# Performance work log

Hardware: AMD Instinct MI355X
Metric: run time of the kernel (lower is better)

Reference implementation:

```python
import jax, jax.numpy as jnp
import numpy as np

# SNNConfig constants (see init_kwargs)
TAU_MEM = 0.02
TAU_SYN = 0.005
DT = 0.001
THRESHOLD = 1.0
BETA = 10.0  # fast-sigmoid surrogate beta

BATCH, TIME, IN_DIM, HIDDEN = 32, 1024, 512, 512


@jax.custom_vjp
def spike_fn(v):
    """Heaviside spike with fast-sigmoid surrogate gradient."""
    return (v > THRESHOLD).astype(v.dtype)


def _spike_fwd(v):
    return spike_fn(v), v


def _spike_bwd(v, g):
    x = v - THRESHOLD
    surr = 1.0 / jnp.square(1.0 + BETA * jnp.abs(x))
    return (g * surr,)


spike_fn.defvjp(_spike_fwd, _spike_bwd)


def setup_inputs() -> dict:
    key = jax.random.key(0)
    k1, k2 = jax.random.split(key)
    spikes = jax.random.uniform(k1, (BATCH, TIME, IN_DIM), dtype=jnp.float32)
    # xavier_uniform for (IN_DIM, HIDDEN)
    limit = np.sqrt(6.0 / (IN_DIM + HIDDEN))
    W = jax.random.uniform(k2, (IN_DIM, HIDDEN), dtype=jnp.float32,
                           minval=-limit, maxval=limit)
    b = jnp.zeros((HIDDEN,), dtype=jnp.float32)
    return {"spikes": spikes, "W": W, "b": b}


def reference(spikes, W, b):
    # spikes: [B, T, I]; W: [I, H]; b: [H]
    alpha_mem = jnp.exp(jnp.asarray(-DT / TAU_MEM, dtype=spikes.dtype))
    alpha_syn = jnp.exp(jnp.asarray(-DT / TAU_SYN, dtype=spikes.dtype))
    # hoist the per-step GEMM into one big contraction: [B, T, H]
    I_in = jnp.einsum('bti,ih->bth', spikes, W) + b

    B, T, H = I_in.shape
    v0 = jnp.zeros((B, H), dtype=spikes.dtype)
    s0 = jnp.zeros((B, H), dtype=spikes.dtype)

    def lif_step(carry, i_t):
        v_mem, i_syn = carry
        i_syn = alpha_syn * i_syn + i_t
        v_mem = alpha_mem * v_mem + i_syn
        out = spike_fn(v_mem)
        v_mem = v_mem - out * THRESHOLD  # soft reset
        return (v_mem, i_syn), out

    _, out_spikes = jax.lax.scan(lif_step, (v0, s0), I_in.transpose(1, 0, 2))
    return out_spikes.transpose(1, 0, 2)  # [B, T, H]
```

## Files before the change

kernel.cpp:

```cpp
#include <hip/hip_runtime.h>
#include <hip/hip_bf16.h>

constexpr int BATCH  = 32;
constexpr int TIME   = 1024;
constexpr int IN_DIM = 512;
constexpr int HIDDEN = 512;

constexpr int GM = BATCH * TIME;
constexpr int GN = HIDDEN;
constexpr int GK = IN_DIM;

#define GLOBAL_AS __attribute__((address_space(1)))
#define LDS_AS    __attribute__((address_space(3)))

#define WAITCNT_VMCNT(n) (((n) & 15) | (((n) >> 4) << 14) | (0x7 << 4) | (0xF << 8))
#define COMPILER_FENCE() asm volatile("" ::: "memory")

constexpr int BM = 128;
constexpr int BN = 128;
constexpr int BK = 16;
constexpr int LDAs = BM + 4;
constexpr int LDBs = BN + 4;

__global__ __launch_bounds__(256) void sgemm_bias_kernel(
    const float* __restrict__ A,
    const float* __restrict__ B,
    const float* __restrict__ bias,
    float* __restrict__ C)
{
    __shared__ __align__(16) float As[BK * LDAs];
    __shared__ __align__(16) float Bs[BK * LDBs];

    const int tid = threadIdx.x;
    const int bm  = blockIdx.x * BM;
    const int bn  = blockIdx.y * BN;

    const int w    = tid >> 6;
    const int lane = tid & 63;
    const int row0 = (w >> 1) * 64 + (lane >> 3) * 8;
    const int col0 = (w & 1)  * 64 + (lane & 7)  * 8;

    const int ar0 = tid >> 2;
    const int ac  = (tid & 3) << 2;
    const int br0 = tid >> 5;
    const int bc  = (tid & 31) << 2;

    float acc[8][8];
    #pragma unroll
    for (int i = 0; i < 8; ++i)
        #pragma unroll
        for (int j = 0; j < 8; ++j) acc[i][j] = 0.0f;

    #pragma unroll 1
    for (int k0 = 0; k0 < GK; k0 += BK) {
        float4 va0 = *reinterpret_cast<const float4*>(A + (size_t)(bm + ar0) * GK + k0 + ac);
        float4 va1 = *reinterpret_cast<const float4*>(A + (size_t)(bm + ar0 + 64) * GK + k0 + ac);
        float4 vb0 = *reinterpret_cast<const float4*>(B + (size_t)(k0 + br0) * GN + bn + bc);
        float4 vb1 = *reinterpret_cast<const float4*>(B + (size_t)(k0 + br0 + 8) * GN + bn + bc);

        __syncthreads();

        As[(ac + 0) * LDAs + ar0] = va0.x;
        As[(ac + 1) * LDAs + ar0] = va0.y;
        As[(ac + 2) * LDAs + ar0] = va0.z;
        As[(ac + 3) * LDAs + ar0] = va0.w;
        As[(ac + 0) * LDAs + ar0 + 64] = va1.x;
        As[(ac + 1) * LDAs + ar0 + 64] = va1.y;
        As[(ac + 2) * LDAs + ar0 + 64] = va1.z;
        As[(ac + 3) * LDAs + ar0 + 64] = va1.w;
        *reinterpret_cast<float4*>(&Bs[br0 * LDBs + bc]) = vb0;
        *reinterpret_cast<float4*>(&Bs[(br0 + 8) * LDBs + bc]) = vb1;

        __syncthreads();

        #pragma unroll
        for (int kk = 0; kk < BK; ++kk) {
            const float4 a0 = *reinterpret_cast<const float4*>(&As[kk * LDAs + row0]);
            const float4 a1 = *reinterpret_cast<const float4*>(&As[kk * LDAs + row0 + 4]);
            const float4 b0 = *reinterpret_cast<const float4*>(&Bs[kk * LDBs + col0]);
            const float4 b1 = *reinterpret_cast<const float4*>(&Bs[kk * LDBs + col0 + 4]);
            const float arr[8] = {a0.x, a0.y, a0.z, a0.w, a1.x, a1.y, a1.z, a1.w};
            const float brr[8] = {b0.x, b0.y, b0.z, b0.w, b1.x, b1.y, b1.z, b1.w};
            #pragma unroll
            for (int i = 0; i < 8; ++i)
                #pragma unroll
                for (int j = 0; j < 8; ++j)
                    acc[i][j] = fmaf(arr[i], brr[j], acc[i][j]);
        }
    }

    #pragma unroll
    for (int i = 0; i < 8; ++i) {
        const size_t r = (size_t)(bm + row0 + i);
        #pragma unroll
        for (int j = 0; j < 8; j += 4) {
            float4 v;
            v.x = __fadd_rn(acc[i][j + 0], bias[bn + col0 + j + 0]);
            v.y = __fadd_rn(acc[i][j + 1], bias[bn + col0 + j + 1]);
            v.z = __fadd_rn(acc[i][j + 2], bias[bn + col0 + j + 2]);
            v.w = __fadd_rn(acc[i][j + 3], bias[bn + col0 + j + 3]);
            *reinterpret_cast<float4*>(&C[r * GN + bn + col0 + j]) = v;
        }
    }
}

constexpr int SH   = 64;
constexpr int SCH  = 16;
constexpr int NCHK = TIME / SCH;
constexpr int RT   = 256;
constexpr int RCH  = RT / SCH;

__global__ __launch_bounds__(128) void lif_scan_kernel(
    const float* __restrict__ I,
    float* __restrict__ O)
{
    __shared__ __align__(16) float ring[RT * SH];
    __shared__ int prod_c;
    __shared__ int cons_c;

    const int blk  = blockIdx.x;
    const int b    = blk >> 3;
    const int h0   = (blk & 7) * SH;
    const int wave = threadIdx.x >> 6;
    const int lane = threadIdx.x & 63;
    const size_t base0 = (size_t)b * TIME * HIDDEN + h0;

    if (threadIdx.x == 0) { prod_c = 0; cons_c = 0; }
    __syncthreads();

    if (wave == 0) {
        const float* g0 = I + base0 + (size_t)(lane >> 4) * HIDDEN + (lane & 15) * 4;
        #pragma unroll 1
        for (int c = 0; c < NCHK; ++c) {
            if (c >= RCH) {
                while (__hip_atomic_load(&cons_c, __ATOMIC_RELAXED,
                                         __HIP_MEMORY_SCOPE_WORKGROUP)
                       < c - RCH + 1) { }
                COMPILER_FENCE();
            }
            const int slot = (c & (RCH - 1)) * SCH;
            #pragma unroll
            for (int u = 0; u < 4; ++u) {
                __builtin_amdgcn_global_load_lds(
                    (GLOBAL_AS const void*)(g0 + (size_t)(c * SCH + u * 4) * HIDDEN),
                    (LDS_AS void*)&ring[(slot + u * 4) * SH], 16, 0, 0);
            }
            COMPILER_FENCE();
            __builtin_amdgcn_s_waitcnt(WAITCNT_VMCNT(16));
            COMPILER_FENCE();
            if (c >= 4)
                __hip_atomic_store(&prod_c, c - 3, __ATOMIC_RELAXED,
                                   __HIP_MEMORY_SCOPE_WORKGROUP);
        }
        COMPILER_FENCE();
        __builtin_amdgcn_s_waitcnt(WAITCNT_VMCNT(0));
        COMPILER_FENCE();
        __hip_atomic_store(&prod_c, NCHK, __ATOMIC_RELAXED,
                           __HIP_MEMORY_SCOPE_WORKGROUP);
    } else {
        const float am = 0.95122942450071400910f;
        const float as = 0.81873075307798185867f;
        float v = 0.0f, s = 0.0f;
        float* o0 = O + base0 + lane;

        #pragma unroll 1
        for (int c = 0; c < NCHK; ++c) {
            while (__hip_atomic_load(&prod_c, __ATOMIC_RELAXED,
                                     __HIP_MEMORY_SCOPE_WORKGROUP) < c + 1) { }
            COMPILER_FENCE();
            const int slot = (c & (RCH - 1)) * SCH;
            float ob[SCH];
            #pragma unroll
            for (int u = 0; u < SCH; ++u) {
                const float x = ring[(slot + u) * SH + lane];
                s = __fadd_rn(__fmul_rn(as, s), x);
                v = __fadd_rn(__fmul_rn(am, v), s);
                const float o = (v > 1.0f) ? 1.0f : 0.0f;
                v = __fsub_rn(v, o);
                ob[u] = o;
            }
            COMPILER_FENCE();
            __hip_atomic_store(&cons_c, c + 1, __ATOMIC_RELAXED,
                               __HIP_MEMORY_SCOPE_WORKGROUP);
            #pragma unroll
            for (int u = 0; u < SCH; ++u)
                o0[(size_t)(c * SCH + u) * HIDDEN] = ob[u];
        }
    }
}

extern "C" void kernel_launch(void* const* d_in, const int* in_sizes, int n_in,
                              void* d_out, int out_size, void* d_ws, size_t ws_size,
                              hipStream_t stream) {
    const float* spikes = (const float*)d_in[0];
    const float* W      = (const float*)d_in[1];
    const float* bias   = (const float*)d_in[2];
    float* out  = (float*)d_out;
    float* I_in = (float*)d_ws;

    dim3 g1(GM / BM, GN / BN);
    sgemm_bias_kernel<<<g1, 256, 0, stream>>>(spikes, W, bias, I_in);

    lif_scan_kernel<<<BATCH * HIDDEN / SH, 128, 0, stream>>>(I_in, out);
}
```

Measured before the change: 307.0 us.

## Use three register-staged producer waves feeding the LIF scan ring buffer

The scan kernel's single producer wave issuing async global-to-LDS loads is replaced by three producer waves. Each handles every third chunk, double-buffers its loads in registers and writes the chunk to the LDS ring with ds stores. Each producer publishes its own progress flag that the consumer polls. The aim is more memory-level parallelism so the serial consumer wave never stalls on data, at the cost of more threads per block, extra registers and more spin-wait traffic.

```diff
diff --git a/kernel.cpp b/kernel.cpp
--- a/kernel.cpp
+++ b/kernel.cpp
@@ -10,10 +10,7 @@
 constexpr int GN = HIDDEN;
 constexpr int GK = IN_DIM;
 
-#define GLOBAL_AS __attribute__((address_space(1)))
-#define LDS_AS    __attribute__((address_space(3)))
-
-#define WAITCNT_VMCNT(n) (((n) & 15) | (((n) >> 4) << 14) | (0x7 << 4) | (0xF << 8))
+#define WAITCNT_LGKMCNT(n) (0xF | (0x7 << 4) | (((n) & 0xF) << 8) | (0x3 << 14))
 #define COMPILER_FENCE() asm volatile("" ::: "memory")
 
 constexpr int BM = 128;
@@ -110,12 +107,12 @@
 constexpr int RT   = 256;
 constexpr int RCH  = RT / SCH;
 
-__global__ __launch_bounds__(128) void lif_scan_kernel(
+__global__ __launch_bounds__(256) void lif_scan_kernel(
     const float* __restrict__ I,
     float* __restrict__ O)
 {
     __shared__ __align__(16) float ring[RT * SH];
-    __shared__ int prod_c;
+    __shared__ int prod_f[3];
     __shared__ int cons_c;
 
     const int blk  = blockIdx.x;
@@ -125,13 +122,28 @@
     const int lane = threadIdx.x & 63;
     const size_t base0 = (size_t)b * TIME * HIDDEN + h0;
 
-    if (threadIdx.x == 0) { prod_c = 0; cons_c = 0; }
+    if (threadIdx.x < 3) prod_f[threadIdx.x] = -1;
+    if (threadIdx.x == 3) cons_c = 0;
     __syncthreads();
 
-    if (wave == 0) {
+    if (wave < 3) {
+        const int p = wave;
         const float* g0 = I + base0 + (size_t)(lane >> 4) * HIDDEN + (lane & 15) * 4;
+
+        float4 rr[2][4];
+        auto loadc = [&](float4* r, int c) {
+            #pragma unroll
+            for (int u = 0; u < 4; ++u)
+                r[u] = *reinterpret_cast<const float4*>(
+                    g0 + (size_t)(c * SCH + u * 4) * HIDDEN);
+        };
+
+        loadc(rr[0], p);
+        int q = 0;
         #pragma unroll 1
-        for (int c = 0; c < NCHK; ++c) {
+        for (int c = p; c < NCHK; c += 3) {
+            const int cn = c + 3;
+            loadc(rr[q ^ 1], (cn < NCHK) ? cn : c);
             if (c >= RCH) {
                 while (__hip_atomic_load(&cons_c, __ATOMIC_RELAXED,
                                          __HIP_MEMORY_SCOPE_WORKGROUP)
@@ -139,24 +151,17 @@
                 COMPILER_FENCE();
             }
             const int slot = (c & (RCH - 1)) * SCH;
-            #pragma unroll
-            for (int u = 0; u < 4; ++u) {
-                __builtin_amdgcn_global_load_lds(
-                    (GLOBAL_AS const void*)(g0 + (size_t)(c * SCH + u * 4) * HIDDEN),
-                    (LDS_AS void*)&ring[(slot + u * 4) * SH], 16, 0, 0);
-            }
-            COMPILER_FENCE();
-            __builtin_amdgcn_s_waitcnt(WAITCNT_VMCNT(16));
-            COMPILER_FENCE();
-            if (c >= 4)
-                __hip_atomic_store(&prod_c, c - 3, __ATOMIC_RELAXED,
-                                   __HIP_MEMORY_SCOPE_WORKGROUP);
-        }
-        COMPILER_FENCE();
-        __builtin_amdgcn_s_waitcnt(WAITCNT_VMCNT(0));
-        COMPILER_FENCE();
-        __hip_atomic_store(&prod_c, NCHK, __ATOMIC_RELAXED,
-                           __HIP_MEMORY_SCOPE_WORKGROUP);
+            float* dst = &ring[(slot + (lane >> 4)) * SH + (lane & 15) * 4];
+            #pragma unroll
+            for (int u = 0; u < 4; ++u)
+                *reinterpret_cast<float4*>(dst + u * 4 * SH) = rr[q][u];
+            COMPILER_FENCE();
+            __builtin_amdgcn_s_waitcnt(WAITCNT_LGKMCNT(0));
+            COMPILER_FENCE();
+            __hip_atomic_store(&prod_f[p], c, __ATOMIC_RELAXED,
+                               __HIP_MEMORY_SCOPE_WORKGROUP);
+            q ^= 1;
+        }
     } else {
         const float am = 0.95122942450071400910f;
         const float as = 0.81873075307798185867f;
@@ -165,8 +170,9 @@
 
         #pragma unroll 1
         for (int c = 0; c < NCHK; ++c) {
-            while (__hip_atomic_load(&prod_c, __ATOMIC_RELAXED,
-                                     __HIP_MEMORY_SCOPE_WORKGROUP) < c + 1) { }
+            const int src = c % 3;
+            while (__hip_atomic_load(&prod_f[src], __ATOMIC_RELAXED,
+                                     __HIP_MEMORY_SCOPE_WORKGROUP) < c) { }
             COMPILER_FENCE();
             const int slot = (c & (RCH - 1)) * SCH;
             float ob[SCH];
@@ -201,5 +207,5 @@
     dim3 g1(GM / BM, GN / BN);
     sgemm_bias_kernel<<<g1, 256, 0, stream>>>(spikes, W, bias, I_in);
 
-    lif_scan_kernel<<<BATCH * HIDDEN / SH, 128, 0, stream>>>(I_in, out);
+    lif_scan_kernel<<<BATCH * HIDDEN / SH, 256, 0, stream>>>(I_in, out);
 }
```

New measurement: 313.4 us. 1.02x slower.
